# Kernel optimization log

Hardware: AMD Instinct MI355X
Metric: run time of the kernel (lower is better)

## Reference

```python
import jax, jax.numpy as jnp
import numpy as np

N = 100000   # nodes
E = 1000000  # edges
G = 1024     # graphs
S = 128      # subgraphs (super-graphs)
NODE = 64    # node feature dim
EDGE = 32    # edge feature dim
H = 64       # hidden size
OUT = 32     # output classes
L = 3        # num GIN layers
BN_EPS = 1e-5


def setup_inputs() -> dict:
    key = jax.random.key(0)
    ks = jax.random.split(key, 32)
    p = lambda k, shape: jax.random.normal(k, shape, jnp.float32) * 0.05
    inp = {
        "x": jax.random.normal(ks[0], (N, NODE), jnp.float32),
        "edge_index": jax.random.randint(ks[1], (2, E), 0, N),
        "edge_attr": jax.random.normal(ks[2], (E, EDGE), jnp.float32),
        "batch": jnp.sort(jax.random.randint(ks[3], (N,), 0, G)),
        "weights": jax.random.uniform(ks[4], (G, 1), jnp.float32, 0.1, 1.0),
        "subgraph_batch": jnp.sort(jax.random.randint(ks[5], (G,), 0, S)),
        # per-layer GINConv params (node_size == hidden_size so layers stack)
        "be_w1": p(ks[6], (L, EDGE, H)), "be_b1": p(ks[7], (L, H)),
        "be_w2": p(ks[8], (L, H, H)),   "be_b2": p(ks[9], (L, H)),
        "mlp_w1": p(ks[10], (L, H, H)), "mlp_b1": p(ks[11], (L, H)),
        "mlp_w2": p(ks[12], (L, H, H)), "mlp_b2": p(ks[13], (L, H)),
        "eps": jnp.zeros((L,), jnp.float32),
        "bn_gamma": jnp.ones((L, H), jnp.float32),
        "bn_beta": jnp.zeros((L, H), jnp.float32),
        "fc0_w": p(ks[14], (L * H, H)), "fc0_b": p(ks[15], (H,)),
        "fc1_w": p(ks[16], (H, H)),     "fc1_b": p(ks[17], (H,)),
        "fc2_w": p(ks[18], (H, H)),     "fc2_b": p(ks[19], (H,)),
        "pred_w": p(ks[20], (H, OUT)),  "pred_b": p(ks[21], (OUT,)),
    }
    return inp


def reference(x, edge_index, edge_attr, batch, weights, subgraph_batch,
              be_w1, be_b1, be_w2, be_b2, mlp_w1, mlp_b1, mlp_w2, mlp_b2,
              eps, bn_gamma, bn_beta, fc0_w, fc0_b, fc1_w, fc1_b,
              fc2_w, fc2_b, pred_w, pred_b):
    src, dst = edge_index[0], edge_index[1]
    n = x.shape[0]
    h = x
    xs = []
    for l in range(be_w1.shape[0]):
        # bond encoder: Linear -> ReLU -> Linear  [E, H]
        e = jnp.maximum(edge_attr @ be_w1[l] + be_b1[l], 0.0) @ be_w2[l] + be_b2[l]
        # message: relu(x_j + edge_emb), aggregate: scatter-add to target nodes
        msg = jnp.maximum(h[src] + e, 0.0)                      # [E, H]
        agg = jax.ops.segment_sum(msg, dst, num_segments=n)     # [N, H]
        z = (1.0 + eps[l]) * h + agg
        # update MLP: Linear -> ReLU -> Linear, then outer ReLU
        z = jnp.maximum(z @ mlp_w1[l] + mlp_b1[l], 0.0) @ mlp_w2[l] + mlp_b2[l]
        z = jnp.maximum(z, 0.0)
        # BatchNorm over nodes (training-mode batch statistics, biased var)
        mu = z.mean(axis=0)
        var = z.var(axis=0)
        z = (z - mu) * jax.lax.rsqrt(var + BN_EPS) * bn_gamma[l] + bn_beta[l]
        h = z
        xs.append(z)
    hc = jnp.concatenate(xs, axis=-1)                           # [N, L*H]
    g_num = weights.shape[0]
    cnt = jax.ops.segment_sum(jnp.ones((n,), hc.dtype), batch, num_segments=g_num)
    g = jax.ops.segment_sum(hc, batch, num_segments=g_num) / jnp.maximum(cnt, 1.0)[:, None]
    g = jnp.maximum(g @ fc0_w + fc0_b, 0.0) * weights           # [G, H]
    s = jax.ops.segment_sum(g, subgraph_batch, num_segments=S)  # [S, H]
    norm = jax.ops.segment_sum(weights, subgraph_batch, num_segments=S)
    s = s / jnp.maximum(norm, 1e-12)
    s = jnp.maximum(s @ fc1_w + fc1_b, 0.0)
    s = jnp.maximum(s @ fc2_w + fc2_b, 0.0)
    return s @ pred_w + pred_b                                  # [S, OUT]
```

## Files before the change

kernel.cpp:

```cpp
#include <hip/hip_runtime.h>

#define NN 100000
#define NE 1000000
#define NG 1024
#define NSG 128
#define EF 32
#define HH 64
#define NOUT 32
#define NL 3
#define NWAVE (NE / 64)

typedef __attribute__((ext_vector_type(8))) short bf16x8;
typedef __attribute__((ext_vector_type(4))) float f32x4;

__device__ __forceinline__ float bcastf(float v, int l) {
    return __int_as_float(__builtin_amdgcn_readlane(__float_as_int(v), l));
}

__device__ __forceinline__ short f2bf(float x) {
    unsigned u = __float_as_uint(x);
    u += 0x7FFFu + ((u >> 16) & 1u);
    return (short)(u >> 16);
}

__device__ __forceinline__ void wave_lds_sync() {
    __builtin_amdgcn_wave_barrier();
    asm volatile("s_waitcnt lgkmcnt(0)" ::: "memory");
    __builtin_amdgcn_wave_barrier();
}

__device__ __forceinline__ void gld16(const float* g, float* l) {
    __builtin_amdgcn_global_load_lds(
        (const __attribute__((address_space(1))) void*)g,
        (__attribute__((address_space(3))) void*)l, 16, 0, 0);
}

__global__ void cnt_kernel(const int* __restrict__ batch, float* __restrict__ cnt) {
    int i = blockIdx.x * blockDim.x + threadIdx.x;
    if (i < NN) atomicAdd(&cnt[batch[i]], 1.0f);
}

__global__ void norm_kernel(const int* __restrict__ sgb, const float* __restrict__ w,
                            float* __restrict__ norm) {
    int i = blockIdx.x * blockDim.x + threadIdx.x;
    if (i < NG) atomicAdd(&norm[sgb[i]], w[i]);
}

__global__ void hist_kernel(const int* __restrict__ eidx, int* __restrict__ off) {
    int e = blockIdx.x * 256 + threadIdx.x;
    if (e < NE) atomicAdd(&off[eidx[NE + e]], 1);
}

__global__ void scan1(int* __restrict__ off, int* __restrict__ bsum) {
    __shared__ int s[256];
    const int i = blockIdx.x * 256 + threadIdx.x;
    const int v = (i < NN) ? off[i] : 0;
    s[threadIdx.x] = v; __syncthreads();
    for (int d = 1; d < 256; d <<= 1) {
        const int t = (threadIdx.x >= d) ? s[threadIdx.x - d] : 0;
        __syncthreads(); s[threadIdx.x] += t; __syncthreads();
    }
    if (i < NN) off[i] = s[threadIdx.x] - v;
    if (threadIdx.x == 255) bsum[blockIdx.x] = s[255];
}

__global__ void scan2(int* __restrict__ bsum, int nb) {
    __shared__ int s[512];
    const int v = (threadIdx.x < nb) ? bsum[threadIdx.x] : 0;
    s[threadIdx.x] = v; __syncthreads();
    for (int d = 1; d < 512; d <<= 1) {
        const int t = (threadIdx.x >= d) ? s[threadIdx.x - d] : 0;
        __syncthreads(); s[threadIdx.x] += t; __syncthreads();
    }
    if (threadIdx.x < nb) bsum[threadIdx.x] = s[threadIdx.x] - v;
}

__global__ void scan3(int* __restrict__ off, const int* __restrict__ bsum) {
    const int i = blockIdx.x * 256 + threadIdx.x;
    if (i < NN) off[i] += bsum[blockIdx.x];
}

__global__ void scatter_kernel(const int* __restrict__ eidx, int* __restrict__ off,
                               int* __restrict__ perm_s, int* __restrict__ src_s,
                               int* __restrict__ dst_s) {
    int e = blockIdx.x * 256 + threadIdx.x;
    if (e < NE) {
        const int d = eidx[NE + e];
        const int p = atomicAdd(&off[d], 1);
        perm_s[p] = e;
        src_s[p]  = eidx[e];
        dst_s[p]  = d;
    }
}

__global__ __launch_bounds__(256, 4) void edge_mfma(
    const float* __restrict__ hin,
    const float* __restrict__ eattr,
    const int*   __restrict__ perm_s,
    const int*   __restrict__ src_s,
    const int*   __restrict__ dst_s,
    const float* __restrict__ w1,
    const float* __restrict__ b1,
    const float* __restrict__ w2,
    const float* __restrict__ b2,
    float*       __restrict__ agg)
{
    __shared__ float ldsall[4][2560];
    const int lane = threadIdx.x & 63;
    const int wv   = threadIdx.x >> 6;
    const int col  = lane & 15;
    const int quad = lane >> 4;
    float* EM = &ldsall[wv][0];
    short* T  = (short*)EM;
    float* HG = &ldsall[wv][1024];
    float* EA = &ldsall[wv][2048];

    const int wid = __builtin_amdgcn_readfirstlane(
        (blockIdx.x * 256 + (int)threadIdx.x) >> 6);
    if (wid >= NWAVE) return;
    const int ebase = wid * 64;

    bf16x8 B1f[4];
    #pragma unroll
    for (int nt = 0; nt < 4; ++nt)
        #pragma unroll
        for (int j = 0; j < 8; ++j)
            B1f[nt][j] = f2bf(w1[(quad * 8 + j) * HH + nt * 16 + col]);
    bf16x8 B2f[2][4];
    #pragma unroll
    for (int ks = 0; ks < 2; ++ks)
        #pragma unroll
        for (int nt = 0; nt < 4; ++nt)
            #pragma unroll
            for (int j = 0; j < 8; ++j)
                B2f[ks][nt][j] = f2bf(w2[(ks * 32 + quad * 8 + j) * HH + nt * 16 + col]);
    float b1v[4], b2v[4];
    #pragma unroll
    for (int nt = 0; nt < 4; ++nt) {
        b1v[nt] = b1[nt * 16 + col];
        b2v[nt] = b2[nt * 16 + col];
    }

    const int sv_all = src_s[ebase + lane];
    const int dv_all = dst_s[ebase + lane];
    const int pe_all = perm_s[ebase + lane];

    const int ea_srcchunk = (lane & 7) ^ ((lane >> 3) & 7);
    const int ea_subrow   = lane >> 3;
    const int hg_subrow   = lane >> 4;
    const int hg_off      = (lane & 15) * 4;

    #define ISSUE_EA(g)                                                        \
        {                                                                      \
            _Pragma("unroll")                                                  \
            for (int b = 0; b < 2; ++b) {                                      \
                const int srow = (g) * 16 + b * 8 + ea_subrow;                 \
                const int pe   = __shfl(pe_all, srow, 64);                     \
                gld16(eattr + (size_t)pe * EF + ea_srcchunk * 4,               \
                      EA + b * 256);                                           \
            }                                                                  \
        }
    #define ISSUE_HG(g)                                                        \
        {                                                                      \
            _Pragma("unroll")                                                  \
            for (int b = 0; b < 4; ++b) {                                      \
                const int srow = (g) * 16 + b * 4 + hg_subrow;                 \
                const int s    = __shfl(sv_all, srow, 64);                     \
                gld16(hin + (size_t)s * HH + hg_off, HG + b * 256);            \
            }                                                                  \
        }

    ISSUE_EA(0);
    ISSUE_HG(0);

    int   cur = -1;
    float acc = 0.0f;

    #pragma unroll
    for (int gi = 0; gi < 4; ++gi) {
        const int gnx = (gi < 3) ? gi + 1 : 3;

        asm volatile("s_waitcnt vmcnt(4)" ::: "memory");

        const int sbase = (2 * quad) ^ (col & 6);
        const float4 fa = *(const float4*)&EA[col * 32 + sbase * 4];
        const float4 fb = *(const float4*)&EA[col * 32 + sbase * 4 + 4];
        const bool odd = (col & 1);
        const float4 lo = odd ? fb : fa;
        const float4 hi = odd ? fa : fb;
        bf16x8 A1;
        A1[0] = f2bf(lo.x); A1[1] = f2bf(lo.y); A1[2] = f2bf(lo.z); A1[3] = f2bf(lo.w);
        A1[4] = f2bf(hi.x); A1[5] = f2bf(hi.y); A1[6] = f2bf(hi.z); A1[7] = f2bf(hi.w);
        wave_lds_sync();
        ISSUE_EA(gnx);

        #pragma unroll
        for (int nt = 0; nt < 4; ++nt) {
            f32x4 C = {0.f, 0.f, 0.f, 0.f};
            C = __builtin_amdgcn_mfma_f32_16x16x32_bf16(A1, B1f[nt], C, 0, 0, 0);
            #pragma unroll
            for (int r = 0; r < 4; ++r) {
                const float tv = fmaxf(C[r] + b1v[nt], 0.0f);
                T[(quad * 4 + r) * 72 + nt * 16 + col] = f2bf(tv);
            }
        }
        wave_lds_sync();

        bf16x8 A2_0 = *(const bf16x8*)&T[col * 72 + 0  + quad * 8];
        bf16x8 A2_1 = *(const bf16x8*)&T[col * 72 + 32 + quad * 8];
        wave_lds_sync();

        #pragma unroll
        for (int nt = 0; nt < 4; ++nt) {
            f32x4 C = {0.f, 0.f, 0.f, 0.f};
            C = __builtin_amdgcn_mfma_f32_16x16x32_bf16(A2_0, B2f[0][nt], C, 0, 0, 0);
            C = __builtin_amdgcn_mfma_f32_16x16x32_bf16(A2_1, B2f[1][nt], C, 0, 0, 0);
            #pragma unroll
            for (int r = 0; r < 4; ++r)
                EM[(quad * 4 + r) * 64 + nt * 16 + col] = C[r] + b2v[nt];
        }
        wave_lds_sync();

        asm volatile("s_waitcnt vmcnt(2)" ::: "memory");

        #pragma unroll
        for (int e2 = 0; e2 < 16; ++e2) {
            const int d = __builtin_amdgcn_readlane(dv_all, gi * 16 + e2);
            const float msg = fmaxf(HG[e2 * 64 + lane] + EM[e2 * 64 + lane], 0.0f);
            if (d != cur) {
                if (cur >= 0) atomicAdd(&agg[(size_t)cur * HH + lane], acc);
                acc = 0.0f; cur = d;
            }
            acc += msg;
        }
        wave_lds_sync();
        ISSUE_HG(gnx);
    }
    if (cur >= 0) atomicAdd(&agg[(size_t)cur * HH + lane], acc);
    #undef ISSUE_EA
    #undef ISSUE_HG
}

__global__ __launch_bounds__(256, 3) void node_fused(
    const float* __restrict__ hin,
    float*       agg,
    const float* __restrict__ w1, const float* __restrict__ b1,
    const float* __restrict__ w2, const float* __restrict__ b2,
    const float* __restrict__ epsp,
    float*       __restrict__ stats)
{
    __shared__ float wlds[2 * HH * HH];
    __shared__ float tb[4][8 * 68];
    {
        const float4* s1 = (const float4*)w1;
        const float4* s2 = (const float4*)w2;
        float4* d = (float4*)wlds;
        for (int i = threadIdx.x; i < 1024; i += 256) d[i] = s1[i];
        for (int i = threadIdx.x; i < 1024; i += 256) d[1024 + i] = s2[i];
    }
    __syncthreads();

    const int lane = threadIdx.x & 63;
    const int wv   = threadIdx.x >> 6;
    float* T = tb[wv];
    const float* w1s = wlds;
    const float* w2s = wlds + HH * HH;

    const int tile = blockIdx.x * 4 + wv;
    const int base = tile * 64;
    if (base >= NN) return;
    const int n = min(base + lane, NN - 1);
    const float epsv = 1.0f + epsp[0];

    float z[HH];
    const float4* hp = (const float4*)(hin + (size_t)n * HH);
    const float4* gp = (const float4*)(agg + (size_t)n * HH);
    #pragma unroll
    for (int c = 0; c < 16; ++c) {
        const float4 h4 = hp[c];
        const float4 g4 = gp[c];
        z[4*c]   = fmaf(epsv, h4.x, g4.x);
        z[4*c+1] = fmaf(epsv, h4.y, g4.y);
        z[4*c+2] = fmaf(epsv, h4.z, g4.z);
        z[4*c+3] = fmaf(epsv, h4.w, g4.w);
    }

    float v[HH];
    #pragma unroll
    for (int k = 0; k < HH; ++k) v[k] = b2[k];

    #pragma unroll 1
    for (int jb = 0; jb < 8; ++jb) {
        const int j0 = jb * 8;
        float t[8];
        #pragma unroll
        for (int q = 0; q < 8; ++q) t[q] = b1[j0 + q];
        #pragma unroll
        for (int i = 0; i < HH; ++i) {
            const float zi = z[i];
            const float4 wA = *(const float4*)&w1s[i * HH + j0];
            const float4 wB = *(const float4*)&w1s[i * HH + j0 + 4];
            t[0] = fmaf(zi, wA.x, t[0]); t[1] = fmaf(zi, wA.y, t[1]);
            t[2] = fmaf(zi, wA.z, t[2]); t[3] = fmaf(zi, wA.w, t[3]);
            t[4] = fmaf(zi, wB.x, t[4]); t[5] = fmaf(zi, wB.y, t[5]);
            t[6] = fmaf(zi, wB.z, t[6]); t[7] = fmaf(zi, wB.w, t[7]);
        }
        #pragma unroll
        for (int q = 0; q < 8; ++q) {
            const float tq = fmaxf(t[q], 0.0f);
            const float* wr = w2s + (j0 + q) * HH;
            #pragma unroll
            for (int kc = 0; kc < 16; ++kc) {
                const float4 wv4 = *(const float4*)&wr[kc * 4];
                v[kc*4+0] = fmaf(tq, wv4.x, v[kc*4+0]);
                v[kc*4+1] = fmaf(tq, wv4.y, v[kc*4+1]);
                v[kc*4+2] = fmaf(tq, wv4.z, v[kc*4+2]);
                v[kc*4+3] = fmaf(tq, wv4.w, v[kc*4+3]);
            }
        }
    }
    #pragma unroll
    for (int k = 0; k < HH; ++k) v[k] = fmaxf(v[k], 0.0f);

    const int valid = min(64, NN - base);
    float s1 = 0.0f, s2 = 0.0f;
    #pragma unroll 1
    for (int cb = 0; cb < 8; ++cb) {
        const int r = lane & 7;
        if ((lane >> 3) == cb && cb * 8 + r < valid) {
            #pragma unroll
            for (int kc = 0; kc < 16; ++kc)
                *(float4*)&T[r * 68 + kc * 4] =
                    float4{v[kc*4], v[kc*4+1], v[kc*4+2], v[kc*4+3]};
        }
        wave_lds_sync();
        const int lim = min(max(valid - cb * 8, 0), 8);
        for (int e2 = 0; e2 < lim; ++e2) {
            const int nn2 = base + cb * 8 + e2;
            const float val = T[e2 * 68 + lane];
            agg[(size_t)nn2 * HH + lane] = val;
            s1 += val;
            s2 += val * val;
        }
        wave_lds_sync();
    }
    atomicAdd(&stats[lane], s1);
    atomicAdd(&stats[64 + lane], s2);
}

__global__ void bn_finalize(float* stats) {
    int j = threadIdx.x;
    if (j < HH) {
        float mu  = stats[j] * (1.0f / NN);
        float var = stats[64 + j] * (1.0f / NN) - mu * mu;
        stats[128 + j] = mu;
        stats[192 + j] = 1.0f / sqrtf(var + 1e-5f);
    }
}

#define CHUNK 32
__global__ void bn_apply(
    const float* __restrict__ v, const float* __restrict__ stats,
    const float* __restrict__ gamma, const float* __restrict__ beta,
    const int* __restrict__ batch,
    float* __restrict__ hout, float* __restrict__ pooled, int layer)
{
    const int lane = threadIdx.x & 63;
    const int wv   = (blockIdx.x * blockDim.x + threadIdx.x) >> 6;
    const int n0   = wv * CHUNK;
    if (n0 >= NN) return;
    const int n1 = min(n0 + CHUNK, NN);
    const float mu = stats[128 + lane], rs = stats[192 + lane];
    const float ga = gamma[lane],       be = beta[lane];
    float acc = 0.0f;
    int cur = batch[n0];
    for (int n = n0; n < n1; ++n) {
        const int b = batch[n];
        const float z = (v[(size_t)n * HH + lane] - mu) * rs * ga + be;
        hout[(size_t)n * HH + lane] = z;
        if (b != cur) {
            atomicAdd(&pooled[(size_t)cur * (NL * HH) + layer * HH + lane], acc);
            acc = 0.0f; cur = b;
        }
        acc += z;
    }
    atomicAdd(&pooled[(size_t)cur * (NL * HH) + layer * HH + lane], acc);
}

__global__ __launch_bounds__(256, 1) void graph_kernel(
    const float* __restrict__ pooled, const float* __restrict__ cnt,
    const float* __restrict__ fc0_w, const float* __restrict__ fc0_b,
    const float* __restrict__ wts, const int* __restrict__ sgb,
    float* __restrict__ s_acc)
{
    __shared__ float w[NL * HH * HH];
    for (int i = threadIdx.x; i < NL * HH * HH; i += blockDim.x) w[i] = fc0_w[i];
    __syncthreads();
    const int lane = threadIdx.x & 63;
    const int g = blockIdx.x * 4 + (threadIdx.x >> 6);
    if (g >= NG) return;
    const float inv = 1.0f / fmaxf(cnt[g], 1.0f);
    float acc = fc0_b[lane];
    #pragma unroll
    for (int c = 0; c < NL; ++c) {
        const float a = pooled[g * (NL * HH) + c * HH + lane] * inv;
        #pragma unroll
        for (int k = 0; k < HH; ++k)
            acc = fmaf(bcastf(a, k), w[(c * HH + k) * HH + lane], acc);
    }
    const float og = fmaxf(acc, 0.0f) * wts[g];
    atomicAdd(&s_acc[sgb[g] * HH + lane], og);
}

__global__ __launch_bounds__(256, 1) void final_kernel(
    const float* __restrict__ s_acc, const float* __restrict__ norm,
    const float* __restrict__ fc1_w, const float* __restrict__ fc1_b,
    const float* __restrict__ fc2_w, const float* __restrict__ fc2_b,
    const float* __restrict__ pw, const float* __restrict__ pb,
    float* __restrict__ out)
{
    const int lane = threadIdx.x & 63;
    const int s = blockIdx.x * 4 + (threadIdx.x >> 6);
    if (s >= NSG) return;
    const float xv = s_acc[s * HH + lane] / fmaxf(norm[s], 1e-12f);
    float u = fc1_b[lane];
    #pragma unroll
    for (int k = 0; k < HH; ++k) u = fmaf(bcastf(xv, k), fc1_w[k * HH + lane], u);
    u = fmaxf(u, 0.0f);
    float v = fc2_b[lane];
    #pragma unroll
    for (int k = 0; k < HH; ++k) v = fmaf(bcastf(u, k), fc2_w[k * HH + lane], v);
    v = fmaxf(v, 0.0f);
    float o = pb[lane & 31];
    #pragma unroll
    for (int k = 0; k < HH; ++k) o = fmaf(bcastf(v, k), pw[k * NOUT + (lane & 31)], o);
    if (lane < NOUT) out[s * NOUT + lane] = o;
}

extern "C" void kernel_launch(void* const* d_in, const int* in_sizes, int n_in,
                              void* d_out, int out_size, void* d_ws, size_t ws_size,
                              hipStream_t stream)
{
    const float* x        = (const float*)d_in[0];
    const int*   eidx     = (const int*)d_in[1];
    const float* eattr    = (const float*)d_in[2];
    const int*   batch    = (const int*)d_in[3];
    const float* weights  = (const float*)d_in[4];
    const int*   sgb      = (const int*)d_in[5];
    const float* be_w1    = (const float*)d_in[6];
    const float* be_b1    = (const float*)d_in[7];
    const float* be_w2    = (const float*)d_in[8];
    const float* be_b2    = (const float*)d_in[9];
    const float* mlp_w1   = (const float*)d_in[10];
    const float* mlp_b1   = (const float*)d_in[11];
    const float* mlp_w2   = (const float*)d_in[12];
    const float* mlp_b2   = (const float*)d_in[13];
    const float* eps      = (const float*)d_in[14];
    const float* bn_gamma = (const float*)d_in[15];
    const float* bn_beta  = (const float*)d_in[16];
    const float* fc0_w    = (const float*)d_in[17];
    const float* fc0_b    = (const float*)d_in[18];
    const float* fc1_w    = (const float*)d_in[19];
    const float* fc1_b    = (const float*)d_in[20];
    const float* fc2_w    = (const float*)d_in[21];
    const float* fc2_b    = (const float*)d_in[22];
    const float* pred_w   = (const float*)d_in[23];
    const float* pred_b   = (const float*)d_in[24];
    float* out = (float*)d_out;

    float* ws     = (float*)d_ws;
    float* h_buf  = ws;
    float* agg    = ws + (size_t)NN * HH;
    float* pooled = ws + (size_t)NN * HH * 2;
    float* cnt    = pooled + (size_t)NG * NL * HH;
    float* stats  = cnt + NG;
    float* s_acc  = stats + 256;
    float* norm   = s_acc + (size_t)NSG * HH;
    int*   ioff   = (int*)(norm + NSG);
    int*   bsum   = ioff + NN;
    int*   perm_s = bsum + 512;
    int*   src_s  = perm_s + NE;
    int*   dst_s  = src_s + NE;

    size_t acc_floats = (size_t)NG * NL * HH + NG + 256 + (size_t)NSG * HH + NSG;
    hipMemsetAsync(pooled, 0, acc_floats * sizeof(float), stream);
    hipMemsetAsync(ioff, 0, NN * sizeof(int), stream);

    const int nb = (NN + 255) / 256;
    hist_kernel<<<(NE + 255) / 256, 256, 0, stream>>>(eidx, ioff);
    scan1<<<nb, 256, 0, stream>>>(ioff, bsum);
    scan2<<<1, 512, 0, stream>>>(bsum, nb);
    scan3<<<nb, 256, 0, stream>>>(ioff, bsum);
    scatter_kernel<<<(NE + 255) / 256, 256, 0, stream>>>(eidx, ioff, perm_s, src_s, dst_s);

    cnt_kernel<<<(NN + 255) / 256, 256, 0, stream>>>(batch, cnt);
    norm_kernel<<<4, 256, 0, stream>>>(sgb, weights, norm);

    const float* hin = x;
    const int eblocks = (NWAVE + 3) / 4;
    const int node_tiles = (NN + 63) / 64;
    const int node_blocks = (node_tiles + 3) / 4;
    const int bn_waves  = (NN + CHUNK - 1) / CHUNK;
    const int bn_blocks = (bn_waves + 3) / 4;
    for (int l = 0; l < NL; ++l) {
        hipMemsetAsync(agg, 0, (size_t)NN * HH * sizeof(float), stream);
        hipMemsetAsync(stats, 0, 256 * sizeof(float), stream);
        edge_mfma<<<eblocks, 256, 0, stream>>>(
            hin, eattr, perm_s, src_s, dst_s,
            be_w1 + l * EF * HH, be_b1 + l * HH,
            be_w2 + l * HH * HH, be_b2 + l * HH, agg);
        node_fused<<<node_blocks, 256, 0, stream>>>(
            hin, agg,
            mlp_w1 + l * HH * HH, mlp_b1 + l * HH,
            mlp_w2 + l * HH * HH, mlp_b2 + l * HH,
            eps + l, stats);
        bn_finalize<<<1, 64, 0, stream>>>(stats);
        bn_apply<<<bn_blocks, 256, 0, stream>>>(
            agg, stats, bn_gamma + l * HH, bn_beta + l * HH,
            batch, h_buf, pooled, l);
        hin = h_buf;
    }

    graph_kernel<<<NG / 4, 256, 0, stream>>>(pooled, cnt, fc0_w, fc0_b,
                                             weights, sgb, s_acc);
    final_kernel<<<NSG / 4, 256, 0, stream>>>(s_acc, norm, fc1_w, fc1_b,
                                              fc2_w, fc2_b, pred_w, pred_b, out);
}
```

Measured before the change: 1.059 ms.

## Cut launches, pad edge LDS rows, read node MLP weights from global

Merges the count and norm kernels into one prep kernel. Folds bn_finalize into bn_apply, and moves the stats buffer next to agg so one memset clears both. In edge_mfma, the EM rows are padded to 68 floats to reduce LDS bank conflicts, and the redundant final-iteration prefetches are skipped behind explicit vmcnt waits and sched barriers. node_fused now reads its weights directly from global/cache rather than staging them in LDS, which removes a block-wide sync and the LDS footprint but may cost bandwidth.

```diff
diff --git a/kernel.cpp b/kernel.cpp
--- a/kernel.cpp
+++ b/kernel.cpp
@@ -35,14 +35,14 @@
         (__attribute__((address_space(3))) void*)l, 16, 0, 0);
 }
 
-__global__ void cnt_kernel(const int* __restrict__ batch, float* __restrict__ cnt) {
+#define WAITVM_(n) asm volatile("s_waitcnt vmcnt(" #n ")" ::: "memory")
+#define WAITVM(n) WAITVM_(n)
+
+__global__ void prep_kernel(const int* __restrict__ batch, const int* __restrict__ sgb,
+                            const float* __restrict__ w,
+                            float* __restrict__ cnt, float* __restrict__ norm) {
     int i = blockIdx.x * blockDim.x + threadIdx.x;
     if (i < NN) atomicAdd(&cnt[batch[i]], 1.0f);
-}
-
-__global__ void norm_kernel(const int* __restrict__ sgb, const float* __restrict__ w,
-                            float* __restrict__ norm) {
-    int i = blockIdx.x * blockDim.x + threadIdx.x;
     if (i < NG) atomicAdd(&norm[sgb[i]], w[i]);
 }
 
@@ -105,15 +105,15 @@
     const float* __restrict__ b2,
     float*       __restrict__ agg)
 {
-    __shared__ float ldsall[4][2560];
+    __shared__ float ldsall[4][2624];
     const int lane = threadIdx.x & 63;
     const int wv   = threadIdx.x >> 6;
     const int col  = lane & 15;
     const int quad = lane >> 4;
     float* EM = &ldsall[wv][0];
     short* T  = (short*)EM;
-    float* HG = &ldsall[wv][1024];
-    float* EA = &ldsall[wv][2048];
+    float* HG = &ldsall[wv][1088];
+    float* EA = &ldsall[wv][2112];
 
     const int wid = __builtin_amdgcn_readfirstlane(
         (blockIdx.x * 256 + (int)threadIdx.x) >> 6);
@@ -170,6 +170,9 @@
             }                                                                  \
         }
 
+    WAITVM(0);
+    __builtin_amdgcn_sched_barrier(0);
+
     ISSUE_EA(0);
     ISSUE_HG(0);
 
@@ -178,9 +181,8 @@
 
     #pragma unroll
     for (int gi = 0; gi < 4; ++gi) {
-        const int gnx = (gi < 3) ? gi + 1 : 3;
-
-        asm volatile("s_waitcnt vmcnt(4)" ::: "memory");
+        WAITVM(4);
+        __builtin_amdgcn_sched_barrier(0);
 
         const int sbase = (2 * quad) ^ (col & 6);
         const float4 fa = *(const float4*)&EA[col * 32 + sbase * 4];
@@ -192,7 +194,7 @@
         A1[0] = f2bf(lo.x); A1[1] = f2bf(lo.y); A1[2] = f2bf(lo.z); A1[3] = f2bf(lo.w);
         A1[4] = f2bf(hi.x); A1[5] = f2bf(hi.y); A1[6] = f2bf(hi.z); A1[7] = f2bf(hi.w);
         wave_lds_sync();
-        ISSUE_EA(gnx);
+        if (gi < 3) ISSUE_EA(gi + 1);
 
         #pragma unroll
         for (int nt = 0; nt < 4; ++nt) {
@@ -217,16 +219,17 @@
             C = __builtin_amdgcn_mfma_f32_16x16x32_bf16(A2_1, B2f[1][nt], C, 0, 0, 0);
             #pragma unroll
             for (int r = 0; r < 4; ++r)
-                EM[(quad * 4 + r) * 64 + nt * 16 + col] = C[r] + b2v[nt];
-        }
-        wave_lds_sync();
-
-        asm volatile("s_waitcnt vmcnt(2)" ::: "memory");
+                EM[(quad * 4 + r) * 68 + nt * 16 + col] = C[r] + b2v[nt];
+        }
+        wave_lds_sync();
+
+        if (gi < 3) { WAITVM(2); } else { WAITVM(0); }
+        __builtin_amdgcn_sched_barrier(0);
 
         #pragma unroll
         for (int e2 = 0; e2 < 16; ++e2) {
             const int d = __builtin_amdgcn_readlane(dv_all, gi * 16 + e2);
-            const float msg = fmaxf(HG[e2 * 64 + lane] + EM[e2 * 64 + lane], 0.0f);
+            const float msg = fmaxf(HG[e2 * 64 + lane] + EM[e2 * 68 + lane], 0.0f);
             if (d != cur) {
                 if (cur >= 0) atomicAdd(&agg[(size_t)cur * HH + lane], acc);
                 acc = 0.0f; cur = d;
@@ -234,7 +237,7 @@
             acc += msg;
         }
         wave_lds_sync();
-        ISSUE_HG(gnx);
+        if (gi < 3) ISSUE_HG(gi + 1);
     }
     if (cur >= 0) atomicAdd(&agg[(size_t)cur * HH + lane], acc);
     #undef ISSUE_EA
@@ -249,22 +252,11 @@
     const float* __restrict__ epsp,
     float*       __restrict__ stats)
 {
-    __shared__ float wlds[2 * HH * HH];
     __shared__ float tb[4][8 * 68];
-    {
-        const float4* s1 = (const float4*)w1;
-        const float4* s2 = (const float4*)w2;
-        float4* d = (float4*)wlds;
-        for (int i = threadIdx.x; i < 1024; i += 256) d[i] = s1[i];
-        for (int i = threadIdx.x; i < 1024; i += 256) d[1024 + i] = s2[i];
-    }
-    __syncthreads();
 
     const int lane = threadIdx.x & 63;
     const int wv   = threadIdx.x >> 6;
     float* T = tb[wv];
-    const float* w1s = wlds;
-    const float* w2s = wlds + HH * HH;
 
     const int tile = blockIdx.x * 4 + wv;
     const int base = tile * 64;
@@ -298,8 +290,8 @@
         #pragma unroll
         for (int i = 0; i < HH; ++i) {
             const float zi = z[i];
-            const float4 wA = *(const float4*)&w1s[i * HH + j0];
-            const float4 wB = *(const float4*)&w1s[i * HH + j0 + 4];
+            const float4 wA = *(const float4*)&w1[i * HH + j0];
+            const float4 wB = *(const float4*)&w1[i * HH + j0 + 4];
             t[0] = fmaf(zi, wA.x, t[0]); t[1] = fmaf(zi, wA.y, t[1]);
             t[2] = fmaf(zi, wA.z, t[2]); t[3] = fmaf(zi, wA.w, t[3]);
             t[4] = fmaf(zi, wB.x, t[4]); t[5] = fmaf(zi, wB.y, t[5]);
@@ -308,7 +300,7 @@
         #pragma unroll
         for (int q = 0; q < 8; ++q) {
             const float tq = fmaxf(t[q], 0.0f);
-            const float* wr = w2s + (j0 + q) * HH;
+            const float* wr = w2 + (j0 + q) * HH;
             #pragma unroll
             for (int kc = 0; kc < 16; ++kc) {
                 const float4 wv4 = *(const float4*)&wr[kc * 4];
@@ -346,16 +338,6 @@
     }
     atomicAdd(&stats[lane], s1);
     atomicAdd(&stats[64 + lane], s2);
-}
-
-__global__ void bn_finalize(float* stats) {
-    int j = threadIdx.x;
-    if (j < HH) {
-        float mu  = stats[j] * (1.0f / NN);
-        float var = stats[64 + j] * (1.0f / NN) - mu * mu;
-        stats[128 + j] = mu;
-        stats[192 + j] = 1.0f / sqrtf(var + 1e-5f);
-    }
 }
 
 #define CHUNK 32
@@ -370,7 +352,9 @@
     const int n0   = wv * CHUNK;
     if (n0 >= NN) return;
     const int n1 = min(n0 + CHUNK, NN);
-    const float mu = stats[128 + lane], rs = stats[192 + lane];
+    const float mu  = stats[lane] * (1.0f / NN);
+    const float var = stats[64 + lane] * (1.0f / NN) - mu * mu;
+    const float rs  = 1.0f / sqrtf(var + 1e-5f);
     const float ga = gamma[lane],       be = beta[lane];
     float acc = 0.0f;
     int cur = batch[n0];
@@ -471,10 +455,10 @@
     float* ws     = (float*)d_ws;
     float* h_buf  = ws;
     float* agg    = ws + (size_t)NN * HH;
-    float* pooled = ws + (size_t)NN * HH * 2;
+    float* stats  = ws + (size_t)NN * HH * 2;
+    float* pooled = stats + 256;
     float* cnt    = pooled + (size_t)NG * NL * HH;
-    float* stats  = cnt + NG;
-    float* s_acc  = stats + 256;
+    float* s_acc  = cnt + NG;
     float* norm   = s_acc + (size_t)NSG * HH;
     int*   ioff   = (int*)(norm + NSG);
     int*   bsum   = ioff + NN;
@@ -482,7 +466,7 @@
     int*   src_s  = perm_s + NE;
     int*   dst_s  = src_s + NE;
 
-    size_t acc_floats = (size_t)NG * NL * HH + NG + 256 + (size_t)NSG * HH + NSG;
+    size_t acc_floats = (size_t)NG * NL * HH + NG + (size_t)NSG * HH + NSG;
     hipMemsetAsync(pooled, 0, acc_floats * sizeof(float), stream);
     hipMemsetAsync(ioff, 0, NN * sizeof(int), stream);
 
@@ -493,8 +477,7 @@
     scan3<<<nb, 256, 0, stream>>>(ioff, bsum);
     scatter_kernel<<<(NE + 255) / 256, 256, 0, stream>>>(eidx, ioff, perm_s, src_s, dst_s);
 
-    cnt_kernel<<<(NN + 255) / 256, 256, 0, stream>>>(batch, cnt);
-    norm_kernel<<<4, 256, 0, stream>>>(sgb, weights, norm);
+    prep_kernel<<<(NN + 255) / 256, 256, 0, stream>>>(batch, sgb, weights, cnt, norm);
 
     const float* hin = x;
     const int eblocks = (NWAVE + 3) / 4;
@@ -503,8 +486,7 @@
     const int bn_waves  = (NN + CHUNK - 1) / CHUNK;
     const int bn_blocks = (bn_waves + 3) / 4;
     for (int l = 0; l < NL; ++l) {
-        hipMemsetAsync(agg, 0, (size_t)NN * HH * sizeof(float), stream);
-        hipMemsetAsync(stats, 0, 256 * sizeof(float), stream);
+        hipMemsetAsync(agg, 0, ((size_t)NN * HH + 256) * sizeof(float), stream);
         edge_mfma<<<eblocks, 256, 0, stream>>>(
             hin, eattr, perm_s, src_s, dst_s,
             be_w1 + l * EF * HH, be_b1 + l * HH,
@@ -514,7 +496,6 @@
             mlp_w1 + l * HH * HH, mlp_b1 + l * HH,
             mlp_w2 + l * HH * HH, mlp_b2 + l * HH,
             eps + l, stats);
-        bn_finalize<<<1, 64, 0, stream>>>(stats);
         bn_apply<<<bn_blocks, 256, 0, stream>>>(
             agg, stats, bn_gamma + l * HH, bn_beta + l * HH,
             batch, h_buf, pooled, l);
```

Result: slower. 1.253 ms (+18.4%).
